# Optimization experiments

Hardware: AMD Instinct MI355X
Metric: run time of the kernel (lower is better)

## Reference

```python
import jax, jax.numpy as jnp
import numpy as np

B, N, FD, D, KS, NR, H, ITERS, L = 64, 1024, 768, 256, 8, 4, 4, 3, 2
TS = KS + NR          # total slots = 12
HD = D // H           # head dim = 64
SCALE = HD ** -0.5


def _ln(x, g, b):
    m = x.mean(-1, keepdims=True)
    v = ((x - m) ** 2).mean(-1, keepdims=True)
    return (x - m) / jnp.sqrt(v + 1e-5) * g + b


def setup_inputs() -> dict:
    key = jax.random.key(0)
    ks = iter(jax.random.split(key, 48))
    rn = lambda s, sc=0.02: jax.random.normal(next(ks), s, jnp.float32) * sc
    d = {}
    d['features'] = jax.random.normal(next(ks), (B, N, FD), jnp.float32)
    d['eps_noise'] = jax.random.normal(next(ks), (B, TS, D), jnp.float32)
    d['in_w'] = rn((FD, D)); d['in_b'] = jnp.zeros((D,))
    d['in_ln_g'] = jnp.ones((D,)); d['in_ln_b'] = jnp.zeros((D,))
    d['ni_g'] = jnp.ones((D,)); d['ni_b'] = jnp.zeros((D,))
    d['slot_mu'] = jax.random.normal(next(ks), (1, TS, D), jnp.float32) * D ** -0.5
    d['slot_log_sigma'] = jnp.zeros((1, TS, D), jnp.float32)
    d['q_w'] = rn((D, D)); d['k_w'] = rn((D, D)); d['v_w'] = rn((D, D))
    d['gru_wih'] = rn((D, 3 * D)); d['gru_whh'] = rn((D, 3 * D))
    d['gru_bih'] = jnp.zeros((3 * D,)); d['gru_bhh'] = jnp.zeros((3 * D,))
    d['ns_g'] = jnp.ones((D,)); d['ns_b'] = jnp.zeros((D,))
    d['ffn_ln_g'] = jnp.ones((D,)); d['ffn_ln_b'] = jnp.zeros((D,))
    d['ffn_w1'] = rn((D, 4 * D)); d['ffn_b1'] = jnp.zeros((4 * D,))
    d['ffn_w2'] = rn((4 * D, D)); d['ffn_b2'] = jnp.zeros((D,))
    d['sel_w1'] = rn((D, D // 2)); d['sel_b1'] = jnp.zeros((D // 2,))
    d['sel_w2'] = rn((D // 2, 2)); d['sel_b2'] = jnp.zeros((2,))
    d['gat_W'] = rn((L, D, D)); d['gat_a'] = rn((L, H, 2 * HD), 0.1)
    d['gat_ln_g'] = jnp.ones((L, D)); d['gat_ln_b'] = jnp.zeros((L, D))
    d['gat_fln_g'] = jnp.ones((L, D)); d['gat_fln_b'] = jnp.zeros((L, D))
    d['gat_fw1'] = rn((L, D, 4 * D)); d['gat_fb1'] = jnp.zeros((L, 4 * D))
    d['gat_fw2'] = rn((L, 4 * D, D)); d['gat_fb2'] = jnp.zeros((L, D))
    return d


def reference(features, eps_noise, in_w, in_b, in_ln_g, in_ln_b, ni_g, ni_b,
              slot_mu, slot_log_sigma, q_w, k_w, v_w,
              gru_wih, gru_whh, gru_bih, gru_bhh, ns_g, ns_b,
              ffn_ln_g, ffn_ln_b, ffn_w1, ffn_b1, ffn_w2, ffn_b2,
              sel_w1, sel_b1, sel_w2, sel_b2,
              gat_W, gat_a, gat_ln_g, gat_ln_b, gat_fln_g, gat_fln_b,
              gat_fw1, gat_fb1, gat_fw2, gat_fb2):
    # ---- slot attention ----
    inputs = _ln(features @ in_w + in_b, in_ln_g, in_ln_b)
    x_n = _ln(inputs, ni_g, ni_b)
    slots = slot_mu + jnp.exp(slot_log_sigma) * eps_noise          # [B,TS,D]
    k = (x_n @ k_w).reshape(B, N, H, HD)
    v = (x_n @ v_w).reshape(B, N, H, HD)
    for _ in range(ITERS):
        sn = _ln(slots, ns_g, ns_b)
        q = (sn @ q_w).reshape(B, TS, H, HD)
        dots = jnp.einsum('bihd,bjhd->bihj', q, k) * SCALE         # [B,TS,H,N]
        attn = jax.nn.softmax(dots.reshape(B, TS * H, N), axis=1).reshape(B, TS, H, N)
        attn_n = (attn + 1e-8) / (attn.sum(-1, keepdims=True) + 1e-8)
        updates = jnp.einsum('bjhd,bihj->bihd', v, attn_n).reshape(B * TS, D)
        h_prev = slots.reshape(B * TS, D)
        gx = updates @ gru_wih + gru_bih
        gh = h_prev @ gru_whh + gru_bhh
        xr, xz, xn = jnp.split(gx, 3, axis=-1)
        hr, hz, hn = jnp.split(gh, 3, axis=-1)
        r = jax.nn.sigmoid(xr + hr)
        z = jax.nn.sigmoid(xz + hz)
        n_ = jnp.tanh(xn + r * hn)
        slots = ((1 - z) * n_ + z * h_prev).reshape(B, TS, D)
        f = _ln(slots, ffn_ln_g, ffn_ln_b)
        slots = slots + jax.nn.gelu(f @ ffn_w1 + ffn_b1, approximate=False) @ ffn_w2 + ffn_b2
    obj = slots[:, :KS]
    # ---- slot selection (eval path: argmax) ----
    logits = jax.nn.relu(obj @ sel_w1 + sel_b1) @ sel_w2 + sel_b2  # [B,KS,2]
    decision = (jnp.argmax(logits, -1) == 1).astype(jnp.float32)
    needed = jnp.maximum(2.0 - decision.sum(-1), 0.0)
    inact = 1.0 - decision
    rank = jnp.cumsum(inact, -1)
    decision = jnp.where((inact > 0) & (rank <= needed[:, None]), 1.0, decision)
    x = obj * decision[..., None]
    # ---- GAT reasoning over slots ----
    mask2d = decision[:, :, None] * decision[:, None, :]           # [B,KS,KS]
    for l in range(L):
        hmat = (_ln(x, gat_ln_g[l], gat_ln_b[l]) @ gat_W[l]).reshape(B, KS, H, HD)
        ei = jnp.einsum('bkhd,hd->bkh', hmat, gat_a[l][:, :HD])
        ej = jnp.einsum('bkhd,hd->bkh', hmat, gat_a[l][:, HD:])
        e = ei[:, :, :, None] + jnp.transpose(ej, (0, 2, 1))[:, None, :, :]  # [B,K,H,K]
        e = jnp.where(e >= 0, e, 0.2 * e)
        e = jnp.where(mask2d[:, :, None, :] == 0, -1e9, e)
        alpha = jax.nn.softmax(e, axis=-1)
        out = jnp.einsum('bkhn,bnhd->bkhd', alpha, hmat).reshape(B, KS, D)
        y = x + out
        f = _ln(y, gat_fln_g[l], gat_fln_b[l])
        x = y + jax.nn.gelu(f @ gat_fw1[l] + gat_fb1[l], approximate=False) @ gat_fw2[l] + gat_fb2[l]
    return x
```

## Files before the change

kernel.cpp:

```cpp
#include <hip/hip_runtime.h>
#include <math.h>

#define Bb 64
#define Nn 1024
#define FDd 768
#define Dd 256
#define KSs 8
#define TSs 12
#define Hh 4
#define HDd 64

typedef __attribute__((ext_vector_type(8))) short bf16x8;
typedef __attribute__((ext_vector_type(4))) float f32x4;

__device__ __forceinline__ ushort f2bf(float x) {
    union { float f; uint u; } v; v.f = x;
    uint r = v.u + 0x7FFFu + ((v.u >> 16) & 1u);
    return (ushort)(r >> 16);
}
__device__ __forceinline__ float bf2f(ushort x) {
    union { uint u; float f; } v; v.u = ((uint)x) << 16;
    return v.f;
}
__device__ __forceinline__ uint pack2(float a, float b) {
    return (uint)f2bf(a) | ((uint)f2bf(b) << 16);
}
__device__ __forceinline__ float waveSum(float v) {
    #pragma unroll
    for (int o = 32; o > 0; o >>= 1) v += __shfl_xor(v, o);
    return v;
}
__device__ __forceinline__ float geluf(float v) {
    return 0.5f * v * (1.f + erff(v * 0.70710678118654752f));
}
__device__ __forceinline__ float sigm(float x) { return 1.f / (1.f + expf(-x)); }

__device__ __forceinline__ void load_af(bf16x8* af, const ushort* Alds, int lda, int lr, int lk)
{
    #pragma unroll
    for (int c = 0; c < 8; c++)
        af[c] = *(const bf16x8*)(Alds + lr * lda + c * 32 + lk * 8);
}

template<int NT, typename F>
__device__ __forceinline__ void mm_stream256(const bf16x8* af,
    const ushort* __restrict__ WT, int n0, int lr, int lk, F&& emit)
{
    const ushort* base = WT + (size_t)(n0 + lr) * 256 + lk * 8;
    bf16x8 bA[8], bB[8], bC[8];
    #pragma unroll
    for (int c = 0; c < 8; c++) bA[c] = *(const bf16x8*)(base + c * 32);
    if (NT > 1) {
        const ushort* nb = base + (size_t)16 * 256;
        #pragma unroll
        for (int c = 0; c < 8; c++) bB[c] = *(const bf16x8*)(nb + c * 32);
    }
    #pragma unroll
    for (int nt = 0; nt < NT; nt++) {
        const bf16x8* bc = (nt % 3 == 0) ? bA : (nt % 3 == 1) ? bB : bC;
        bf16x8* bn = (nt % 3 == 0) ? bC : (nt % 3 == 1) ? bA : bB;
        if (nt + 2 < NT) {
            const ushort* nb = base + (size_t)(nt + 2) * 16 * 256;
            #pragma unroll
            for (int c = 0; c < 8; c++) bn[c] = *(const bf16x8*)(nb + c * 32);
        }
        f32x4 a0 = {0.f, 0.f, 0.f, 0.f}, a1 = {0.f, 0.f, 0.f, 0.f};
        #pragma unroll
        for (int c = 0; c < 8; c += 2) a0 = __builtin_amdgcn_mfma_f32_16x16x32_bf16(af[c], bc[c], a0, 0, 0, 0);
        #pragma unroll
        for (int c = 1; c < 8; c += 2) a1 = __builtin_amdgcn_mfma_f32_16x16x32_bf16(af[c], bc[c], a1, 0, 0, 0);
        emit(nt, a0 + a1);
    }
}

template<int NT2, typename F>
__device__ __forceinline__ void mm_stream_1024(const ushort* Alds, int lda,
    const ushort* __restrict__ WT, int n0, int lr, int lk, F&& emit)
{
    f32x4 acc[NT2] = {};
    bf16x8 bA[8], bB[8], bC[8];
    {
        const ushort* nb = WT + (size_t)(n0 + lr) * 1024 + lk * 8;
        #pragma unroll
        for (int c = 0; c < 8; c++) bA[c] = *(const bf16x8*)(nb + c * 32);
    }
    if (4 * NT2 > 1) {
        const int kc1 = 1 / NT2, nt1 = 1 % NT2;
        const ushort* nb = WT + (size_t)(n0 + nt1 * 16 + lr) * 1024 + kc1 * 256 + lk * 8;
        #pragma unroll
        for (int c = 0; c < 8; c++) bB[c] = *(const bf16x8*)(nb + c * 32);
    }
    #pragma unroll
    for (int kc = 0; kc < 4; kc++) {
        bf16x8 af[8];
        #pragma unroll
        for (int c = 0; c < 8; c++)
            af[c] = *(const bf16x8*)(Alds + lr * lda + kc * 256 + c * 32 + lk * 8);
        #pragma unroll
        for (int nt = 0; nt < NT2; nt++) {
            const int step = kc * NT2 + nt;
            const bf16x8* bc = (step % 3 == 0) ? bA : (step % 3 == 1) ? bB : bC;
            bf16x8* bn = (step % 3 == 0) ? bC : (step % 3 == 1) ? bA : bB;
            if (step + 2 < 4 * NT2) {
                const int kc2 = (step + 2) / NT2, nt2 = (step + 2) % NT2;
                const ushort* nb = WT + (size_t)(n0 + nt2 * 16 + lr) * 1024 + kc2 * 256 + lk * 8;
                #pragma unroll
                for (int c = 0; c < 8; c++) bn[c] = *(const bf16x8*)(nb + c * 32);
            }
            #pragma unroll
            for (int c = 0; c < 8; c++)
                acc[nt] = __builtin_amdgcn_mfma_f32_16x16x32_bf16(af[c], bc[c], acc[nt], 0, 0, 0);
        }
    }
    #pragma unroll
    for (int nt = 0; nt < NT2; nt++) emit(nt, acc[nt]);
}

__device__ __forceinline__ void ln_row_bf(const float* __restrict__ rowF,
    ushort* __restrict__ rowU, const float* __restrict__ g,
    const float* __restrict__ b, int lane)
{
    float4 x = *(const float4*)&rowF[lane * 4];
    float m = waveSum(x.x + x.y + x.z + x.w) * (1.f / 256.f);
    float d0 = x.x - m, d1 = x.y - m, d2 = x.z - m, d3 = x.w - m;
    float v = waveSum(d0 * d0 + d1 * d1 + d2 * d2 + d3 * d3) * (1.f / 256.f);
    float inv = 1.f / sqrtf(v + 1e-5f);
    float4 gg = *(const float4*)&g[lane * 4];
    float4 bb = *(const float4*)&b[lane * 4];
    ushort4 o;
    o.x = f2bf(d0 * inv * gg.x + bb.x); o.y = f2bf(d1 * inv * gg.y + bb.y);
    o.z = f2bf(d2 * inv * gg.z + bb.z); o.w = f2bf(d3 * inv * gg.w + bb.w);
    *(ushort4*)&rowU[lane * 4] = o;
}

#define LPAD 40
template<bool A_F32, bool DO_LN>
__global__ __launch_bounds__(256) void gemm_mfma(const void* __restrict__ Ap,
    const ushort* __restrict__ WTa, const ushort* __restrict__ WTb,
    const float* __restrict__ bias,
    const float* __restrict__ g1, const float* __restrict__ b1,
    const float* __restrict__ g2, const float* __restrict__ b2,
    ushort* __restrict__ Ca, ushort* __restrict__ Cb, int M, int K)
{
    constexpr int SMEM_USHORTS = DO_LN ? (64 * 264) : (64 * LPAD + 256 * LPAD);
    __shared__ __align__(16) ushort smem[SMEM_USHORTS];
    ushort* As = smem;
    ushort* Bs = smem + 64 * LPAD;
    ushort* xS = smem;
    const ushort* WT = blockIdx.y ? WTb : WTa;
    ushort* C = blockIdx.y ? Cb : Ca;
    const int t = threadIdx.x;
    const int m0 = blockIdx.x * 64;
    const int lane = t & 63, wv = t >> 6;
    const int lr = lane & 15, lk = lane >> 4;

    f32x4 acc[4][4] = {};

    const float*  agf = (const float*)Ap  + (size_t)(m0 + (t >> 2)) * K + (t & 3) * 8;
    const ushort* agb = (const ushort*)Ap + (size_t)(m0 + (t >> 2)) * K + (t & 3) * 8;
    const ushort* bg  = WT + (size_t)(t >> 2) * K + (t & 3) * 8;

    float4 fA0, fA1; int4 iA0; int4 iB0, iB1, iB2, iB3;

#define GLOAD(k0) do { \
        if (A_F32) { \
            fA0 = *(const float4*)(agf + (k0)); fA1 = *(const float4*)(agf + (k0) + 4); \
        } else { \
            iA0 = *(const int4*)(agb + (k0)); \
        } \
        iB0 = *(const int4*)(bg + (k0)); \
        iB1 = *(const int4*)(bg + (size_t)64  * K + (k0)); \
        iB2 = *(const int4*)(bg + (size_t)128 * K + (k0)); \
        iB3 = *(const int4*)(bg + (size_t)192 * K + (k0)); \
    } while (0)

#define LSTORE() do { \
        if (A_F32) { \
            int4 w; \
            w.x = pack2(fA0.x, fA0.y); w.y = pack2(fA0.z, fA0.w); \
            w.z = pack2(fA1.x, fA1.y); w.w = pack2(fA1.z, fA1.w); \
            *(int4*)&As[(t >> 2) * LPAD + (t & 3) * 8] = w; \
        } else { \
            *(int4*)&As[(t >> 2) * LPAD + (t & 3) * 8] = iA0; \
        } \
        *(int4*)&Bs[(t >> 2) * LPAD + (t & 3) * 8]         = iB0; \
        *(int4*)&Bs[(64 + (t >> 2)) * LPAD + (t & 3) * 8]  = iB1; \
        *(int4*)&Bs[(128 + (t >> 2)) * LPAD + (t & 3) * 8] = iB2; \
        *(int4*)&Bs[(192 + (t >> 2)) * LPAD + (t & 3) * 8] = iB3; \
    } while (0)

    GLOAD(0);
    for (int k0 = 0; k0 < K; k0 += 32) {
        LSTORE();
        __syncthreads();
        bf16x8 af[4], bfr[4];
        #pragma unroll
        for (int mi = 0; mi < 4; mi++)
            af[mi] = *(const bf16x8*)&As[(mi * 16 + lr) * LPAD + lk * 8];
        #pragma unroll
        for (int ni = 0; ni < 4; ni++)
            bfr[ni] = *(const bf16x8*)&Bs[(wv * 64 + ni * 16 + lr) * LPAD + lk * 8];
        if (k0 + 32 < K) GLOAD(k0 + 32);
        #pragma unroll
        for (int mi = 0; mi < 4; mi++)
            #pragma unroll
            for (int ni = 0; ni < 4; ni++)
                acc[mi][ni] = __builtin_amdgcn_mfma_f32_16x16x32_bf16(af[mi], bfr[ni], acc[mi][ni], 0, 0, 0);
        __syncthreads();
    }
#undef GLOAD
#undef LSTORE
    if (DO_LN) {
        #pragma unroll
        for (int mi = 0; mi < 4; mi++) {
            int row = mi * 16 + lk * 4;
            #pragma unroll
            for (int ni = 0; ni < 4; ni++) {
                int col = wv * 64 + ni * 16 + lr;
                float bv = bias[col];
                #pragma unroll
                for (int r = 0; r < 4; r++)
                    xS[(row + r) * 264 + col] = f2bf(acc[mi][ni][r] + bv);
            }
        }
        __syncthreads();
        #pragma unroll
        for (int rr = 0; rr < 16; rr++) {
            int row = wv * 16 + rr;
            ushort4 u = *(const ushort4*)&xS[row * 264 + lane * 4];
            float x0 = bf2f(u.x), x1 = bf2f(u.y), x2 = bf2f(u.z), x3 = bf2f(u.w);
            float m = waveSum(x0 + x1 + x2 + x3) * (1.f / 256.f);
            float d0 = x0 - m, d1 = x1 - m, d2 = x2 - m, d3 = x3 - m;
            float v = waveSum(d0 * d0 + d1 * d1 + d2 * d2 + d3 * d3) * (1.f / 256.f);
            float inv = 1.f / sqrtf(v + 1e-5f);
            float4 gg = *(const float4*)&g1[lane * 4];
            float4 bbv = *(const float4*)&b1[lane * 4];
            float y0 = d0 * inv * gg.x + bbv.x, y1 = d1 * inv * gg.y + bbv.y;
            float y2 = d2 * inv * gg.z + bbv.z, y3 = d3 * inv * gg.w + bbv.w;
            float m2 = waveSum(y0 + y1 + y2 + y3) * (1.f / 256.f);
            float e0 = y0 - m2, e1 = y1 - m2, e2 = y2 - m2, e3 = y3 - m2;
            float v2 = waveSum(e0 * e0 + e1 * e1 + e2 * e2 + e3 * e3) * (1.f / 256.f);
            float inv2 = 1.f / sqrtf(v2 + 1e-5f);
            float4 g2v = *(const float4*)&g2[lane * 4];
            float4 b2v = *(const float4*)&b2[lane * 4];
            ushort4 o;
            o.x = f2bf(e0 * inv2 * g2v.x + b2v.x); o.y = f2bf(e1 * inv2 * g2v.y + b2v.y);
            o.z = f2bf(e2 * inv2 * g2v.z + b2v.z); o.w = f2bf(e3 * inv2 * g2v.w + b2v.w);
            *(ushort4*)&xS[row * 264 + lane * 4] = o;
        }
        __syncthreads();
        for (int idx = t; idx < 4096; idx += 256) {
            int row = idx >> 6, cg = (idx & 63) * 4;
            *(ushort4*)&C[(size_t)(m0 + row) * 256 + cg] =
                *(const ushort4*)&xS[row * 264 + cg];
        }
    } else {
        #pragma unroll
        for (int mi = 0; mi < 4; mi++) {
            int grow = m0 + mi * 16 + lk * 4;
            #pragma unroll
            for (int ni = 0; ni < 4; ni++) {
                int gcol = wv * 64 + ni * 16 + lr;
                float bv = bias ? bias[gcol] : 0.f;
                #pragma unroll
                for (int r = 0; r < 4; r++)
                    C[(size_t)(grow + r) * 256 + gcol] = f2bf(acc[mi][ni][r] + bv);
            }
        }
    }
}

struct PrepArgsT {
    const float* src[14];
    ushort* dst[14];
    int K[14];
    int N[14];
    int tstart[15];
};
__global__ __launch_bounds__(256) void prep_tiled(PrepArgsT pa)
{
    __shared__ float s[32][33];
    int tile = blockIdx.x;
    int seg = 0;
    while (tile >= pa.tstart[seg + 1]) seg++;
    int lt = tile - pa.tstart[seg];
    int K = pa.K[seg], N = pa.N[seg];
    int tpr = N >> 5;
    int k0 = (lt / tpr) << 5, n0 = (lt % tpr) << 5;
    const float* src = pa.src[seg];
    ushort* dst = pa.dst[seg];
    int r = threadIdx.x >> 5, c = threadIdx.x & 31;
    #pragma unroll
    for (int rr = 0; rr < 32; rr += 8)
        s[rr + r][c] = src[(size_t)(k0 + rr + r) * N + n0 + c];
    __syncthreads();
    #pragma unroll
    for (int rr = 0; rr < 32; rr += 8)
        dst[(size_t)(n0 + rr + r) * K + k0 + c] = f2bf(s[c][rr + r]);
}

__global__ __launch_bounds__(512) void slot_init_q(
    const float* __restrict__ mu, const float* __restrict__ ls,
    const float* __restrict__ eps, float* __restrict__ slots_g,
    float* __restrict__ qbuf, const ushort* __restrict__ qwT,
    const float* __restrict__ ns_g, const float* __restrict__ ns_b)
{
    __shared__ float sF[16 * 256];
    __shared__ __align__(16) ushort sU[16 * 264];
    int b = blockIdx.x, t = threadIdx.x;
    int lane = t & 63, wv = t >> 6, lr = lane & 15, lk = lane >> 4;
    for (int idx = t; idx < 4096; idx += 512) {
        int i = idx >> 8, c = idx & 255;
        float v = 0.f;
        if (i < 12) {
            int md = i * 256 + c;
            v = mu[md] + expf(ls[md]) * eps[(size_t)(b * 12 + i) * 256 + c];
            slots_g[(size_t)(b * 12 + i) * 256 + c] = v;
        }
        sF[idx] = v;
        sU[i * 264 + c] = 0;
    }
    __syncthreads();
    ln_row_bf(sF + wv * 256, sU + wv * 264, ns_g, ns_b, lane);
    if (wv < 4) ln_row_bf(sF + (8 + wv) * 256, sU + (8 + wv) * 264, ns_g, ns_b, lane);
    __syncthreads();
    bf16x8 af[8];
    load_af(af, sU, 264, lr, lk);
    mm_stream256<2>(af, qwT, wv * 32, lr, lk, [&](int nt, f32x4 a) {
        int n = wv * 32 + nt * 16 + lr;
        #pragma unroll
        for (int r = 0; r < 4; r++) {
            int m = lk * 4 + r;
            if (m < 12) qbuf[(size_t)(b * 12 + m) * 256 + n] = a[r] * 0.125f;
        }
    });
}

__global__ __launch_bounds__(256) void dots_softmax(const float* __restrict__ qb,
    const ushort* __restrict__ kb, ushort* __restrict__ attnb)
{
    int b = blockIdx.x >> 2, chunk = blockIdx.x & 3;
    int t = threadIdx.x;
    int j = chunk * 256 + t;
    const float* qbase = qb + (size_t)b * 12 * 256;
    float a48[48];
    #pragma unroll
    for (int h = 0; h < 4; h++) {
        const uint* kp = (const uint*)(kb + (size_t)(b * Nn + j) * 256 + h * 64);
        float kr[64];
        #pragma unroll
        for (int c = 0; c < 8; c++) {
            int4 k4 = *(const int4*)(kp + c * 4);
            uint u0 = (uint)k4.x, u1 = (uint)k4.y, u2 = (uint)k4.z, u3 = (uint)k4.w;
            kr[c * 8 + 0] = __uint_as_float(u0 << 16); kr[c * 8 + 1] = __uint_as_float(u0 & 0xffff0000u);
            kr[c * 8 + 2] = __uint_as_float(u1 << 16); kr[c * 8 + 3] = __uint_as_float(u1 & 0xffff0000u);
            kr[c * 8 + 4] = __uint_as_float(u2 << 16); kr[c * 8 + 5] = __uint_as_float(u2 & 0xffff0000u);
            kr[c * 8 + 6] = __uint_as_float(u3 << 16); kr[c * 8 + 7] = __uint_as_float(u3 & 0xffff0000u);
        }
        #pragma unroll
        for (int i = 0; i < 12; i++) {
            const float* qr = qbase + i * 256 + h * 64;
            float acc = 0.f;
            #pragma unroll
            for (int c = 0; c < 64; c++) acc += kr[c] * qr[c];
            a48[i * 4 + h] = acc;
        }
    }
    float m = -1e30f;
    #pragma unroll
    for (int idx = 0; idx < 48; idx++) m = fmaxf(m, a48[idx]);
    float s = 0.f;
    #pragma unroll
    for (int idx = 0; idx < 48; idx++) { a48[idx] = expf(a48[idx] - m); s += a48[idx]; }
    float inv = 1.f / s;
    #pragma unroll
    for (int idx = 0; idx < 48; idx++)
        attnb[(size_t)(b * 48 + idx) * Nn + j] = f2bf(a48[idx] * inv);
}

__global__ __launch_bounds__(512) void updates_kernel(const ushort* __restrict__ attnb,
    const ushort* __restrict__ vb, float* __restrict__ upd)
{
    int b = blockIdx.x >> 2, h = blockIdx.x & 3;
    int t = threadIdx.x, w = t >> 6, lane = t & 63;
    int jj = lane >> 3, dg = lane & 7;
    float acc[12][8] = {};
    float ra[12] = {};
    float accv[8] = {};
    for (int jb = w * 8; jb < Nn; jb += 64) {
        int j = jb + jj;
        bf16x8 v8 = *(const bf16x8*)&vb[(size_t)(b * Nn + j) * Dd + h * HDd + dg * 8];
        float vv[8];
        #pragma unroll
        for (int r = 0; r < 8; r++) { vv[r] = bf2f((ushort)v8[r]); accv[r] += vv[r]; }
        #pragma unroll
        for (int i = 0; i < 12; i++) {
            float a = bf2f(attnb[(size_t)(b * 48 + i * 4 + h) * Nn + j]);
            #pragma unroll
            for (int r = 0; r < 8; r++) acc[i][r] += a * vv[r];
            ra[i] += a;
        }
    }
    #pragma unroll
    for (int i = 0; i < 12; i++) {
        #pragma unroll
        for (int r = 0; r < 8; r++) {
            acc[i][r] += __shfl_xor(acc[i][r], 8);
            acc[i][r] += __shfl_xor(acc[i][r], 16);
            acc[i][r] += __shfl_xor(acc[i][r], 32);
        }
        ra[i] += __shfl_xor(ra[i], 8);
        ra[i] += __shfl_xor(ra[i], 16);
        ra[i] += __shfl_xor(ra[i], 32);
    }
    #pragma unroll
    for (int r = 0; r < 8; r++) {
        accv[r] += __shfl_xor(accv[r], 8);
        accv[r] += __shfl_xor(accv[r], 16);
        accv[r] += __shfl_xor(accv[r], 32);
    }
    __shared__ float redA[8][12][64];
    __shared__ float redV[8][64];
    __shared__ float redR[8][12];
    if (lane < 8) {
        #pragma unroll
        for (int i = 0; i < 12; i++)
            #pragma unroll
            for (int r = 0; r < 8; r++)
                redA[w][i][lane * 8 + r] = acc[i][r];
        #pragma unroll
        for (int r = 0; r < 8; r++) redV[w][lane * 8 + r] = accv[r];
        if (lane == 0) {
            #pragma unroll
            for (int i = 0; i < 12; i++) redR[w][i] = ra[i];
        }
    }
    __syncthreads();
    if (w == 0) {
        float sv = 0.f;
        #pragma unroll
        for (int ww = 0; ww < 8; ww++) sv += redV[ww][lane];
        #pragma unroll
        for (int i = 0; i < 12; i++) {
            float s = 0.f, rs = 0.f;
            #pragma unroll
            for (int ww = 0; ww < 8; ww++) { s += redA[ww][i][lane]; rs += redR[ww][i]; }
            upd[(size_t)(b * TSs + i) * Dd + h * HDd + lane] = (s + 1e-8f * sv) / (rs + 1e-8f);
        }
    }
}

__global__ __launch_bounds__(256) void gru_mm(const float* __restrict__ upd,
    const float* __restrict__ slots_g,
    const ushort* __restrict__ wihT, const ushort* __restrict__ whhT,
    const float* __restrict__ bih, const float* __restrict__ bhh,
    float* __restrict__ gxh)
{
    __shared__ __align__(16) ushort sU[16 * 264], sS[16 * 264];
    int b = blockIdx.x, q = blockIdx.y, t = threadIdx.x;
    int lane = t & 63, wv = t >> 6, lr = lane & 15, lk = lane >> 4;
    for (int idx = t; idx < 4096; idx += 256) {
        int i = idx >> 8, c = idx & 255;
        float uv = 0.f, sv = 0.f;
        if (i < 12) {
            uv = upd[(size_t)(b * 12 + i) * 256 + c];
            sv = slots_g[(size_t)(b * 12 + i) * 256 + c];
        }
        sU[i * 264 + c] = f2bf(uv);
        sS[i * 264 + c] = f2bf(sv);
    }
    __syncthreads();
    bool ih = (wv < 2);
    bf16x8 af[8];
    load_af(af, ih ? sU : sS, 264, lr, lk);
    const ushort* W = ih ? wihT : whhT;
    const float* bias = ih ? bih : bhh;
    float* outp = gxh + (size_t)(b * 2 + (ih ? 0 : 1)) * 12 * 768;
    int n0 = q * 192 + (wv & 1) * 96;
    mm_stream256<6>(af, W, n0, lr, lk, [&](int nt, f32x4 a) {
        int n = n0 + nt * 16 + lr;
        float bv = bias[n];
        #pragma unroll
        for (int r = 0; r < 4; r++) {
            int m = lk * 4 + r;
            if (m < 12) outp[m * 768 + n] = a[r] + bv;
        }
    });
}

__global__ __launch_bounds__(256) void gate_ffn1(const float* __restrict__ gxh,
    const float* __restrict__ slots_g, float* __restrict__ slots2,
    const ushort* __restrict__ fw1T,
    const float* __restrict__ fln_g, const float* __restrict__ fln_b,
    const float* __restrict__ f_b1, ushort* __restrict__ h1b)
{
    __shared__ float sF[12 * 256];
    __shared__ __align__(16) ushort sU[16 * 264];
    int b = blockIdx.x, q = blockIdx.y, t = threadIdx.x;
    int lane = t & 63, wv = t >> 6, lr = lane & 15, lk = lane >> 4;
    for (int idx = t; idx < 1056; idx += 256) sU[12 * 264 + idx] = 0;
    for (int idx = t; idx < 3072; idx += 256) {
        int i = idx >> 8, c = idx & 255;
        const float* gx = gxh + (size_t)(b * 2) * 12 * 768 + i * 768;
        const float* gh = gxh + (size_t)(b * 2 + 1) * 12 * 768 + i * 768;
        float r = sigm(gx[c] + gh[c]);
        float z = sigm(gx[256 + c] + gh[256 + c]);
        float nv = tanhf(gx[512 + c] + r * gh[512 + c]);
        float hp = slots_g[(size_t)(b * 12 + i) * 256 + c];
        float out = (1.f - z) * nv + z * hp;
        sF[idx] = out;
        if (q == 0) slots2[(size_t)(b * 12 + i) * 256 + c] = out;
    }
    __syncthreads();
    for (int rr = 0; rr < 3; rr++) {
        int row = wv * 3 + rr;
        ln_row_bf(sF + row * 256, sU + row * 264, fln_g, fln_b, lane);
    }
    __syncthreads();
    bf16x8 af[8];
    load_af(af, sU, 264, lr, lk);
    int n0 = q * 256 + wv * 64;
    mm_stream256<4>(af, fw1T, n0, lr, lk, [&](int nt, f32x4 a) {
        int n = n0 + nt * 16 + lr;
        float bv = f_b1[n];
        #pragma unroll
        for (int r = 0; r < 4; r++) {
            int m = lk * 4 + r;
            if (m < 12) h1b[(size_t)(b * 12 + m) * 1024 + n] = f2bf(geluf(a[r] + bv));
        }
    });
}

__global__ __launch_bounds__(256) void ffn2_mm(const ushort* __restrict__ h1b,
    const float* __restrict__ slots2, float* __restrict__ slots_g,
    const ushort* __restrict__ fw2T, const float* __restrict__ f_b2)
{
    __shared__ __align__(16) ushort hS[16 * 1032];
    int b = blockIdx.x, q = blockIdx.y, t = threadIdx.x;
    int lane = t & 63, wv = t >> 6, lr = lane & 15, lk = lane >> 4;
    for (int ch = t; ch < 2048; ch += 256) {
        int i = ch >> 7, c8 = (ch & 127) * 8;
        int4 v = {0, 0, 0, 0};
        if (i < 12) v = *(const int4*)&h1b[(size_t)(b * 12 + i) * 1024 + c8];
        *(int4*)&hS[i * 1032 + c8] = v;
    }
    __syncthreads();
    int n0 = q * 64 + wv * 16;
    mm_stream_1024<1>(hS, 1032, fw2T, n0, lr, lk, [&](int nt, f32x4 a) {
        (void)nt;
        int n = n0 + lr;
        float bv = f_b2[n];
        #pragma unroll
        for (int r = 0; r < 4; r++) {
            int m = lk * 4 + r;
            if (m < 12)
                slots_g[(size_t)(b * 12 + m) * 256 + n] =
                    a[r] + bv + slots2[(size_t)(b * 12 + m) * 256 + n];
        }
    });
}

__global__ __launch_bounds__(512) void ln_q(const float* __restrict__ slots_g,
    float* __restrict__ qbuf, const ushort* __restrict__ qwT,
    const float* __restrict__ ns_g, const float* __restrict__ ns_b)
{
    __shared__ float sF[12 * 256];
    __shared__ __align__(16) ushort sU[16 * 264];
    int b = blockIdx.x, t = threadIdx.x;
    int lane = t & 63, wv = t >> 6, lr = lane & 15, lk = lane >> 4;
    for (int idx = t; idx < 3072; idx += 512) sF[idx] = slots_g[(size_t)b * 3072 + idx];
    for (int idx = t; idx < 1056; idx += 512) sU[12 * 264 + idx] = 0;
    __syncthreads();
    ln_row_bf(sF + wv * 256, sU + wv * 264, ns_g, ns_b, lane);
    if (wv < 4) ln_row_bf(sF + (8 + wv) * 256, sU + (8 + wv) * 264, ns_g, ns_b, lane);
    __syncthreads();
    bf16x8 af[8];
    load_af(af, sU, 264, lr, lk);
    mm_stream256<2>(af, qwT, wv * 32, lr, lk, [&](int nt, f32x4 a) {
        int n = wv * 32 + nt * 16 + lr;
        #pragma unroll
        for (int r = 0; r < 4; r++) {
            int m = lk * 4 + r;
            if (m < 12) qbuf[(size_t)(b * 12 + m) * 256 + n] = a[r] * 0.125f;
        }
    });
}

__global__ __launch_bounds__(256) void select_kernel(const float* __restrict__ slots,
    const float* __restrict__ w1, const float* __restrict__ b1,
    const float* __restrict__ w2, const float* __restrict__ b2,
    float* __restrict__ dec, float* __restrict__ xout)
{
    int b = blockIdx.x, t = threadIdx.x;
    __shared__ float t1[8][128];
    __shared__ float lg[8][2];
    __shared__ float dsh[8];
    const float* obj = slots + (size_t)b * TSs * Dd;
    #pragma unroll
    for (int u = 0; u < 4; u++) {
        int idx = t + 256 * u;
        int k = idx >> 7, c = idx & 127;
        float s = b1[c];
        for (int d = 0; d < 256; d++) s += obj[k * 256 + d] * w1[d * 128 + c];
        t1[k][c] = fmaxf(s, 0.f);
    }
    __syncthreads();
    if (t < 16) {
        int k = t >> 1, o = t & 1;
        float s = b2[o];
        for (int c = 0; c < 128; c++) s += t1[k][c] * w2[c * 2 + o];
        lg[k][o] = s;
    }
    __syncthreads();
    if (t == 0) {
        float dv[8]; float sum = 0.f;
        for (int k = 0; k < 8; k++) { dv[k] = (lg[k][1] > lg[k][0]) ? 1.f : 0.f; sum += dv[k]; }
        float needed = fmaxf(2.f - sum, 0.f);
        float rank = 0.f;
        for (int k = 0; k < 8; k++) {
            float inact = 1.f - dv[k];
            rank += inact;
            if (inact > 0.f && rank <= needed) dv[k] = 1.f;
            dsh[k] = dv[k];
            dec[b * 8 + k] = dv[k];
        }
    }
    __syncthreads();
    for (int idx = t; idx < 2048; idx += 256) {
        int k = idx >> 8, c = idx & 255;
        xout[(size_t)(b * 8 + k) * 256 + c] = obj[k * 256 + c] * dsh[k];
    }
}

__global__ __launch_bounds__(256) void gat_attn(const float* __restrict__ xin,
    const float* __restrict__ dec, const ushort* __restrict__ gWT,
    const float* __restrict__ av,
    const float* __restrict__ lng, const float* __restrict__ lnb,
    const float* __restrict__ flng, const float* __restrict__ flnb,
    float* __restrict__ yF, ushort* __restrict__ ylnb)
{
    __shared__ float xF[8 * 256];
    __shared__ float hmF[8 * 256];
    __shared__ __align__(16) ushort sU[16 * 264];
    __shared__ float ei[8][4], ej[8][4], al[8][4][8], ds[8];
    int b = blockIdx.x, t = threadIdx.x;
    int lane = t & 63, wv = t >> 6, lr = lane & 15, lk = lane >> 4;

    for (int idx = t; idx < 2048; idx += 256) xF[idx] = xin[(size_t)b * 2048 + idx];
    for (int idx = t; idx < 2112; idx += 256) sU[8 * 264 + idx] = 0;
    if (t < 8) ds[t] = dec[b * 8 + t];
    __syncthreads();
    ln_row_bf(xF + (wv * 2) * 256, sU + (wv * 2) * 264, lng, lnb, lane);
    ln_row_bf(xF + (wv * 2 + 1) * 256, sU + (wv * 2 + 1) * 264, lng, lnb, lane);
    __syncthreads();
    {
        bf16x8 af[8];
        load_af(af, sU, 264, lr, lk);
        mm_stream256<4>(af, gWT, wv * 64, lr, lk, [&](int nt, f32x4 a) {
            int n = wv * 64 + nt * 16 + lr;
            #pragma unroll
            for (int r = 0; r < 4; r++) {
                int m = lk * 4 + r;
                if (m < 8) hmF[m * 256 + n] = a[r];
            }
        });
    }
    __syncthreads();
    {
        int pair = t >> 3, sub = t & 7;
        int k = pair >> 2, h = pair & 3;
        const float* hrow = hmF + k * 256 + h * 64 + sub * 8;
        float s1 = 0.f, s2 = 0.f;
        #pragma unroll
        for (int d = 0; d < 8; d++) {
            float hv = hrow[d];
            s1 += hv * av[h * 128 + sub * 8 + d];
            s2 += hv * av[h * 128 + 64 + sub * 8 + d];
        }
        #pragma unroll
        for (int o = 1; o < 8; o <<= 1) { s1 += __shfl_xor(s1, o); s2 += __shfl_xor(s2, o); }
        if (sub == 0) { ei[k][h] = s1; ej[k][h] = s2; }
    }
    __syncthreads();
    {
        int k = t >> 5, h = (t >> 3) & 3, n = t & 7;
        float e = ei[k][h] + ej[n][h];
        e = (e >= 0.f) ? e : 0.2f * e;
        if (ds[k] * ds[n] == 0.f) e = -1e9f;
        float mx = e;
        #pragma unroll
        for (int o = 4; o > 0; o >>= 1) mx = fmaxf(mx, __shfl_xor(mx, o, 8));
        float ex = expf(e - mx);
        float sm = ex;
        #pragma unroll
        for (int o = 4; o > 0; o >>= 1) sm += __shfl_xor(sm, o, 8);
        al[k][h][n] = ex / sm;
    }
    __syncthreads();
    {
        int h = t >> 6, d = t & 63;
        #pragma unroll
        for (int k = 0; k < 8; k++) {
            float o = 0.f;
            #pragma unroll
            for (int n = 0; n < 8; n++) o += al[k][h][n] * hmF[n * 256 + h * 64 + d];
            xF[k * 256 + h * 64 + d] += o;
        }
    }
    __syncthreads();
    for (int idx = t; idx < 2048; idx += 256) yF[(size_t)b * 2048 + idx] = xF[idx];
    ln_row_bf(xF + (wv * 2) * 256, sU + (wv * 2) * 264, flng, flnb, lane);
    ln_row_bf(xF + (wv * 2 + 1) * 256, sU + (wv * 2 + 1) * 264, flng, flnb, lane);
    __syncthreads();
    for (int idx = t; idx < 2048; idx += 256) {
        int i = idx >> 8, c = idx & 255;
        ylnb[(size_t)b * 2048 + idx] = sU[i * 264 + c];
    }
}

__global__ __launch_bounds__(256) void gat_ffn1(const ushort* __restrict__ ylnb,
    const ushort* __restrict__ g1T, const float* __restrict__ fb1,
    ushort* __restrict__ gh1)
{
    __shared__ __align__(16) ushort sU[16 * 264];
    int b = blockIdx.x, q = blockIdx.y, t = threadIdx.x;
    int lane = t & 63, wv = t >> 6, lr = lane & 15, lk = lane >> 4;
    for (int idx = t; idx < 4096; idx += 256) {
        int i = idx >> 8, c = idx & 255;
        sU[i * 264 + c] = (i < 8) ? ylnb[(size_t)b * 2048 + i * 256 + c] : 0;
    }
    __syncthreads();
    bf16x8 af[8];
    load_af(af, sU, 264, lr, lk);
    int n0 = q * 256 + wv * 64;
    mm_stream256<4>(af, g1T, n0, lr, lk, [&](int nt, f32x4 a) {
        int n = n0 + nt * 16 + lr;
        float bv = fb1[n];
        #pragma unroll
        for (int r = 0; r < 4; r++) {
            int m = lk * 4 + r;
            if (m < 8) gh1[(size_t)(b * 8 + m) * 1024 + n] = f2bf(geluf(a[r] + bv));
        }
    });
}

__global__ __launch_bounds__(256) void gat_ffn2(const ushort* __restrict__ gh1,
    const float* __restrict__ yF, const ushort* __restrict__ g2T,
    const float* __restrict__ fb2, float* __restrict__ out)
{
    __shared__ __align__(16) ushort hS[16 * 1032];
    int b = blockIdx.x, q = blockIdx.y, t = threadIdx.x;
    int lane = t & 63, wv = t >> 6, lr = lane & 15, lk = lane >> 4;
    for (int ch = t; ch < 2048; ch += 256) {
        int i = ch >> 7, c8 = (ch & 127) * 8;
        int4 v = {0, 0, 0, 0};
        if (i < 8) v = *(const int4*)&gh1[(size_t)(b * 8 + i) * 1024 + c8];
        *(int4*)&hS[i * 1032 + c8] = v;
    }
    __syncthreads();
    int n0 = q * 64 + wv * 16;
    mm_stream_1024<1>(hS, 1032, g2T, n0, lr, lk, [&](int nt, f32x4 a) {
        (void)nt;
        int n = n0 + lr;
        float bv = fb2[n];
        #pragma unroll
        for (int r = 0; r < 4; r++) {
            int m = lk * 4 + r;
            if (m < 8) out[(size_t)(b * 8 + m) * 256 + n] = a[r] + bv + yF[(size_t)(b * 8 + m) * 256 + n];
        }
    });
}

extern "C" void kernel_launch(void* const* d_in, const int* in_sizes, int n_in,
                              void* d_out, int out_size, void* d_ws, size_t ws_size,
                              hipStream_t stream)
{
    (void)in_sizes; (void)n_in; (void)out_size; (void)ws_size;
    const float* features       = (const float*)d_in[0];
    const float* eps_noise      = (const float*)d_in[1];
    const float* in_w           = (const float*)d_in[2];
    const float* in_b           = (const float*)d_in[3];
    const float* in_ln_g        = (const float*)d_in[4];
    const float* in_ln_b        = (const float*)d_in[5];
    const float* ni_g           = (const float*)d_in[6];
    const float* ni_b           = (const float*)d_in[7];
    const float* slot_mu        = (const float*)d_in[8];
    const float* slot_log_sigma = (const float*)d_in[9];
    const float* q_w            = (const float*)d_in[10];
    const float* k_w            = (const float*)d_in[11];
    const float* v_w            = (const float*)d_in[12];
    const float* gru_wih        = (const float*)d_in[13];
    const float* gru_whh        = (const float*)d_in[14];
    const float* gru_bih        = (const float*)d_in[15];
    const float* gru_bhh        = (const float*)d_in[16];
    const float* ns_g           = (const float*)d_in[17];
    const float* ns_b           = (const float*)d_in[18];
    const float* ffn_ln_g       = (const float*)d_in[19];
    const float* ffn_ln_b       = (const float*)d_in[20];
    const float* ffn_w1         = (const float*)d_in[21];
    const float* ffn_b1         = (const float*)d_in[22];
    const float* ffn_w2         = (const float*)d_in[23];
    const float* ffn_b2         = (const float*)d_in[24];
    const float* sel_w1         = (const float*)d_in[25];
    const float* sel_b1         = (const float*)d_in[26];
    const float* sel_w2         = (const float*)d_in[27];
    const float* sel_b2         = (const float*)d_in[28];
    const float* gat_W          = (const float*)d_in[29];
    const float* gat_a          = (const float*)d_in[30];
    const float* gat_ln_g       = (const float*)d_in[31];
    const float* gat_ln_b       = (const float*)d_in[32];
    const float* gat_fln_g      = (const float*)d_in[33];
    const float* gat_fln_b      = (const float*)d_in[34];
    const float* gat_fw1        = (const float*)d_in[35];
    const float* gat_fb1        = (const float*)d_in[36];
    const float* gat_fw2        = (const float*)d_in[37];
    const float* gat_fb2        = (const float*)d_in[38];

    ushort* kb  = (ushort*)d_ws;
    ushort* vb  = kb + 16777216;
    ushort* xnb = vb + 16777216;
    ushort* wtb = xnb + 16777216;
    ushort* h1b  = wtb + 2490368;
    ushort* ylnb = h1b + 786432;
    ushort* gh1  = ylnb + 131072;
    ushort* attnb = gh1 + 524288;
    float* fbase = (float*)(attnb + 3145728);
    float* slots  = fbase;
    float* slots2 = slots + 196608;
    float* qbuf   = slots2 + 196608;
    float* upd    = qbuf + 196608;
    float* gxh    = upd + 196608;
    float* xb     = gxh + 1179648;
    float* yF     = xb + 131072;
    float* dec    = yF + 131072;

    ushort* in_wT = wtb;
    ushort* k_wT  = in_wT + 196608;
    ushort* v_wT  = k_wT + 65536;
    ushort* q_wT  = v_wT + 65536;
    ushort* wihT  = q_wT + 65536;
    ushort* whhT  = wihT + 196608;
    ushort* fw1T  = whhT + 196608;
    ushort* fw2T  = fw1T + 262144;
    ushort* gW0T  = fw2T + 262144;
    ushort* gW1T  = gW0T + 65536;
    ushort* gf1aT = gW1T + 65536;
    ushort* gf1bT = gf1aT + 262144;
    ushort* gf2aT = gf1bT + 262144;
    ushort* gf2bT = gf2aT + 262144;

    dim3 blk(256);

    PrepArgsT pa;
    const float* srcs[14] = { in_w, k_w, v_w, q_w, gru_wih, gru_whh, ffn_w1, ffn_w2,
                              gat_W, gat_W + 65536, gat_fw1, gat_fw1 + 262144,
                              gat_fw2, gat_fw2 + 262144 };
    ushort* dsts[14] = { in_wT, k_wT, v_wT, q_wT, wihT, whhT, fw1T, fw2T,
                         gW0T, gW1T, gf1aT, gf1bT, gf2aT, gf2bT };
    int Ks[14]  = { 768, 256, 256, 256, 256, 256, 256, 1024, 256, 256, 256, 256, 1024, 1024 };
    int Nsz[14] = { 256, 256, 256, 256, 768, 768, 1024, 256, 256, 256, 1024, 1024, 256, 256 };
    int tcum = 0;
    for (int s = 0; s < 14; s++) {
        pa.src[s] = srcs[s]; pa.dst[s] = dsts[s]; pa.K[s] = Ks[s]; pa.N[s] = Nsz[s];
        pa.tstart[s] = tcum;
        tcum += (Ks[s] >> 5) * (Nsz[s] >> 5);
    }
    pa.tstart[14] = tcum;
    prep_tiled<<<tcum, blk, 0, stream>>>(pa);

    gemm_mfma<true, true><<<dim3(1024, 1), blk, 0, stream>>>(
        features, in_wT, nullptr, in_b, in_ln_g, in_ln_b, ni_g, ni_b,
        xnb, nullptr, Bb * Nn, 768);

    gemm_mfma<false, false><<<dim3(1024, 2), blk, 0, stream>>>(
        xnb, k_wT, v_wT, nullptr, nullptr, nullptr, nullptr, nullptr,
        kb, vb, Bb * Nn, 256);

    slot_init_q<<<Bb, dim3(512), 0, stream>>>(slot_mu, slot_log_sigma, eps_noise,
                                              slots, qbuf, q_wT, ns_g, ns_b);

    for (int it = 0; it < 3; it++) {
        dots_softmax<<<Bb * 4, blk, 0, stream>>>(qbuf, kb, attnb);
        updates_kernel<<<Bb * Hh, dim3(512), 0, stream>>>(attnb, vb, upd);
        gru_mm<<<dim3(Bb, 4), blk, 0, stream>>>(upd, slots, wihT, whhT,
                                                gru_bih, gru_bhh, gxh);
        gate_ffn1<<<dim3(Bb, 4), blk, 0, stream>>>(gxh, slots, slots2, fw1T,
                                                   ffn_ln_g, ffn_ln_b, ffn_b1, h1b);
        ffn2_mm<<<dim3(Bb, 4), blk, 0, stream>>>(h1b, slots2, slots, fw2T, ffn_b2);
        if (it < 2)
            ln_q<<<Bb, dim3(512), 0, stream>>>(slots, qbuf, q_wT, ns_g, ns_b);
    }

    select_kernel<<<Bb, blk, 0, stream>>>(slots, sel_w1, sel_b1, sel_w2, sel_b2, dec, xb);

    for (int l = 0; l < 2; l++) {
        const ushort* gWT = l ? gW1T : gW0T;
        const ushort* g1T = l ? gf1bT : gf1aT;
        const ushort* g2T = l ? gf2bT : gf2aT;
        gat_attn<<<Bb, blk, 0, stream>>>(xb, dec, gWT, gat_a + l * 512,
            gat_ln_g + l * 256, gat_ln_b + l * 256,
            gat_fln_g + l * 256, gat_fln_b + l * 256, yF, ylnb);
        gat_ffn1<<<dim3(Bb, 4), blk, 0, stream>>>(ylnb, g1T, gat_fb1 + l * 1024, gh1);
        gat_ffn2<<<dim3(Bb, 4), blk, 0, stream>>>(gh1, yF, g2T, gat_fb2 + l * 256,
            l ? (float*)d_out : xb);
    }
}
```

Before: 567.0 us.

## Fuse input projection, double layernorm, and K/V projections into one kernel

The input-projection GEMM with its two layernorms and the K/V projection GEMM now run in a single kernel. The normalized 64x256 tile stays in shared memory and is multiplied directly by the K and V weights, which are read from global memory with register double-buffering. This removes the round trip of the normalized activation buffer through global memory and one kernel launch. In exchange, each block re-streams the full K and V weight matrices without LDS staging, and register pressure rises.

```diff
diff --git a/kernel.cpp b/kernel.cpp
--- a/kernel.cpp
+++ b/kernel.cpp
@@ -134,21 +134,19 @@
 }
 
 #define LPAD 40
-template<bool A_F32, bool DO_LN>
-__global__ __launch_bounds__(256) void gemm_mfma(const void* __restrict__ Ap,
-    const ushort* __restrict__ WTa, const ushort* __restrict__ WTb,
+__global__ __launch_bounds__(256) void inproj_kv(const float* __restrict__ Ap,
+    const ushort* __restrict__ WT,
+    const ushort* __restrict__ kwT, const ushort* __restrict__ vwT,
     const float* __restrict__ bias,
     const float* __restrict__ g1, const float* __restrict__ b1,
     const float* __restrict__ g2, const float* __restrict__ b2,
-    ushort* __restrict__ Ca, ushort* __restrict__ Cb, int M, int K)
-{
-    constexpr int SMEM_USHORTS = DO_LN ? (64 * 264) : (64 * LPAD + 256 * LPAD);
-    __shared__ __align__(16) ushort smem[SMEM_USHORTS];
+    ushort* __restrict__ kb, ushort* __restrict__ vb)
+{
+    constexpr int K = 768;
+    __shared__ __align__(16) ushort smem[64 * 264];
     ushort* As = smem;
     ushort* Bs = smem + 64 * LPAD;
     ushort* xS = smem;
-    const ushort* WT = blockIdx.y ? WTb : WTa;
-    ushort* C = blockIdx.y ? Cb : Ca;
     const int t = threadIdx.x;
     const int m0 = blockIdx.x * 64;
     const int lane = t & 63, wv = t >> 6;
@@ -156,18 +154,13 @@
 
     f32x4 acc[4][4] = {};
 
-    const float*  agf = (const float*)Ap  + (size_t)(m0 + (t >> 2)) * K + (t & 3) * 8;
-    const ushort* agb = (const ushort*)Ap + (size_t)(m0 + (t >> 2)) * K + (t & 3) * 8;
+    const float*  agf = Ap + (size_t)(m0 + (t >> 2)) * K + (t & 3) * 8;
     const ushort* bg  = WT + (size_t)(t >> 2) * K + (t & 3) * 8;
 
-    float4 fA0, fA1; int4 iA0; int4 iB0, iB1, iB2, iB3;
+    float4 fA0, fA1; int4 iB0, iB1, iB2, iB3;
 
 #define GLOAD(k0) do { \
-        if (A_F32) { \
-            fA0 = *(const float4*)(agf + (k0)); fA1 = *(const float4*)(agf + (k0) + 4); \
-        } else { \
-            iA0 = *(const int4*)(agb + (k0)); \
-        } \
+        fA0 = *(const float4*)(agf + (k0)); fA1 = *(const float4*)(agf + (k0) + 4); \
         iB0 = *(const int4*)(bg + (k0)); \
         iB1 = *(const int4*)(bg + (size_t)64  * K + (k0)); \
         iB2 = *(const int4*)(bg + (size_t)128 * K + (k0)); \
@@ -175,14 +168,10 @@
     } while (0)
 
 #define LSTORE() do { \
-        if (A_F32) { \
-            int4 w; \
-            w.x = pack2(fA0.x, fA0.y); w.y = pack2(fA0.z, fA0.w); \
-            w.z = pack2(fA1.x, fA1.y); w.w = pack2(fA1.z, fA1.w); \
-            *(int4*)&As[(t >> 2) * LPAD + (t & 3) * 8] = w; \
-        } else { \
-            *(int4*)&As[(t >> 2) * LPAD + (t & 3) * 8] = iA0; \
-        } \
+        int4 w; \
+        w.x = pack2(fA0.x, fA0.y); w.y = pack2(fA0.z, fA0.w); \
+        w.z = pack2(fA1.x, fA1.y); w.w = pack2(fA1.z, fA1.w); \
+        *(int4*)&As[(t >> 2) * LPAD + (t & 3) * 8] = w; \
         *(int4*)&Bs[(t >> 2) * LPAD + (t & 3) * 8]         = iB0; \
         *(int4*)&Bs[(64 + (t >> 2)) * LPAD + (t & 3) * 8]  = iB1; \
         *(int4*)&Bs[(128 + (t >> 2)) * LPAD + (t & 3) * 8] = iB2; \
@@ -210,62 +199,73 @@
     }
 #undef GLOAD
 #undef LSTORE
-    if (DO_LN) {
-        #pragma unroll
-        for (int mi = 0; mi < 4; mi++) {
-            int row = mi * 16 + lk * 4;
-            #pragma unroll
-            for (int ni = 0; ni < 4; ni++) {
-                int col = wv * 64 + ni * 16 + lr;
-                float bv = bias[col];
+    #pragma unroll
+    for (int mi = 0; mi < 4; mi++) {
+        int row = mi * 16 + lk * 4;
+        #pragma unroll
+        for (int ni = 0; ni < 4; ni++) {
+            int col = wv * 64 + ni * 16 + lr;
+            float bv = bias[col];
+            #pragma unroll
+            for (int r = 0; r < 4; r++)
+                xS[(row + r) * 264 + col] = f2bf(acc[mi][ni][r] + bv);
+        }
+    }
+    __syncthreads();
+    #pragma unroll
+    for (int rr = 0; rr < 16; rr++) {
+        int row = wv * 16 + rr;
+        ushort4 u = *(const ushort4*)&xS[row * 264 + lane * 4];
+        float x0 = bf2f(u.x), x1 = bf2f(u.y), x2 = bf2f(u.z), x3 = bf2f(u.w);
+        float m = waveSum(x0 + x1 + x2 + x3) * (1.f / 256.f);
+        float d0 = x0 - m, d1 = x1 - m, d2 = x2 - m, d3 = x3 - m;
+        float v = waveSum(d0 * d0 + d1 * d1 + d2 * d2 + d3 * d3) * (1.f / 256.f);
+        float inv = 1.f / sqrtf(v + 1e-5f);
+        float4 gg = *(const float4*)&g1[lane * 4];
+        float4 bbv = *(const float4*)&b1[lane * 4];
+        float y0 = d0 * inv * gg.x + bbv.x, y1 = d1 * inv * gg.y + bbv.y;
+        float y2 = d2 * inv * gg.z + bbv.z, y3 = d3 * inv * gg.w + bbv.w;
+        float m2 = waveSum(y0 + y1 + y2 + y3) * (1.f / 256.f);
+        float e0 = y0 - m2, e1 = y1 - m2, e2 = y2 - m2, e3 = y3 - m2;
+        float v2 = waveSum(e0 * e0 + e1 * e1 + e2 * e2 + e3 * e3) * (1.f / 256.f);
+        float inv2 = 1.f / sqrtf(v2 + 1e-5f);
+        float4 g2v = *(const float4*)&g2[lane * 4];
+        float4 b2v = *(const float4*)&b2[lane * 4];
+        ushort4 o;
+        o.x = f2bf(e0 * inv2 * g2v.x + b2v.x); o.y = f2bf(e1 * inv2 * g2v.y + b2v.y);
+        o.z = f2bf(e2 * inv2 * g2v.z + b2v.z); o.w = f2bf(e3 * inv2 * g2v.w + b2v.w);
+        *(ushort4*)&xS[row * 264 + lane * 4] = o;
+    }
+    __syncthreads();
+    bf16x8 af2[8];
+    load_af(af2, xS + (wv * 16) * 264, 264, lr, lk);
+    #pragma unroll
+    for (int wsel = 0; wsel < 2; wsel++) {
+        const ushort* W = wsel ? vwT : kwT;
+        ushort* outp = wsel ? vb : kb;
+        bf16x8 bufA[8], bufB[8];
+        {
+            const ushort* nb = W + (size_t)lr * 256 + lk * 8;
+            #pragma unroll
+            for (int c = 0; c < 8; c++) bufA[c] = *(const bf16x8*)(nb + c * 32);
+        }
+        #pragma unroll
+        for (int nt = 0; nt < 16; nt++) {
+            const bf16x8* cur = (nt & 1) ? bufB : bufA;
+            bf16x8* nxt = (nt & 1) ? bufA : bufB;
+            if (nt + 1 < 16) {
+                const ushort* nb = W + (size_t)((nt + 1) * 16 + lr) * 256 + lk * 8;
                 #pragma unroll
-                for (int r = 0; r < 4; r++)
-                    xS[(row + r) * 264 + col] = f2bf(acc[mi][ni][r] + bv);
+                for (int c = 0; c < 8; c++) nxt[c] = *(const bf16x8*)(nb + c * 32);
             }
-        }
-        __syncthreads();
-        #pragma unroll
-        for (int rr = 0; rr < 16; rr++) {
-            int row = wv * 16 + rr;
-            ushort4 u = *(const ushort4*)&xS[row * 264 + lane * 4];
-            float x0 = bf2f(u.x), x1 = bf2f(u.y), x2 = bf2f(u.z), x3 = bf2f(u.w);
-            float m = waveSum(x0 + x1 + x2 + x3) * (1.f / 256.f);
-            float d0 = x0 - m, d1 = x1 - m, d2 = x2 - m, d3 = x3 - m;
-            float v = waveSum(d0 * d0 + d1 * d1 + d2 * d2 + d3 * d3) * (1.f / 256.f);
-            float inv = 1.f / sqrtf(v + 1e-5f);
-            float4 gg = *(const float4*)&g1[lane * 4];
-            float4 bbv = *(const float4*)&b1[lane * 4];
-            float y0 = d0 * inv * gg.x + bbv.x, y1 = d1 * inv * gg.y + bbv.y;
-            float y2 = d2 * inv * gg.z + bbv.z, y3 = d3 * inv * gg.w + bbv.w;
-            float m2 = waveSum(y0 + y1 + y2 + y3) * (1.f / 256.f);
-            float e0 = y0 - m2, e1 = y1 - m2, e2 = y2 - m2, e3 = y3 - m2;
-            float v2 = waveSum(e0 * e0 + e1 * e1 + e2 * e2 + e3 * e3) * (1.f / 256.f);
-            float inv2 = 1.f / sqrtf(v2 + 1e-5f);
-            float4 g2v = *(const float4*)&g2[lane * 4];
-            float4 b2v = *(const float4*)&b2[lane * 4];
-            ushort4 o;
-            o.x = f2bf(e0 * inv2 * g2v.x + b2v.x); o.y = f2bf(e1 * inv2 * g2v.y + b2v.y);
-            o.z = f2bf(e2 * inv2 * g2v.z + b2v.z); o.w = f2bf(e3 * inv2 * g2v.w + b2v.w);
-            *(ushort4*)&xS[row * 264 + lane * 4] = o;
-        }
-        __syncthreads();
-        for (int idx = t; idx < 4096; idx += 256) {
-            int row = idx >> 6, cg = (idx & 63) * 4;
-            *(ushort4*)&C[(size_t)(m0 + row) * 256 + cg] =
-                *(const ushort4*)&xS[row * 264 + cg];
-        }
-    } else {
-        #pragma unroll
-        for (int mi = 0; mi < 4; mi++) {
-            int grow = m0 + mi * 16 + lk * 4;
-            #pragma unroll
-            for (int ni = 0; ni < 4; ni++) {
-                int gcol = wv * 64 + ni * 16 + lr;
-                float bv = bias ? bias[gcol] : 0.f;
-                #pragma unroll
-                for (int r = 0; r < 4; r++)
-                    C[(size_t)(grow + r) * 256 + gcol] = f2bf(acc[mi][ni][r] + bv);
-            }
+            f32x4 a = {0.f, 0.f, 0.f, 0.f};
+            #pragma unroll
+            for (int c = 0; c < 8; c++)
+                a = __builtin_amdgcn_mfma_f32_16x16x32_bf16(af2[c], cur[c], a, 0, 0, 0);
+            int n = nt * 16 + lr;
+            #pragma unroll
+            for (int r = 0; r < 4; r++)
+                outp[(size_t)(m0 + wv * 16 + lk * 4 + r) * 256 + n] = f2bf(a[r]);
         }
     }
 }
@@ -868,13 +868,8 @@
     pa.tstart[14] = tcum;
     prep_tiled<<<tcum, blk, 0, stream>>>(pa);
 
-    gemm_mfma<true, true><<<dim3(1024, 1), blk, 0, stream>>>(
-        features, in_wT, nullptr, in_b, in_ln_g, in_ln_b, ni_g, ni_b,
-        xnb, nullptr, Bb * Nn, 768);
-
-    gemm_mfma<false, false><<<dim3(1024, 2), blk, 0, stream>>>(
-        xnb, k_wT, v_wT, nullptr, nullptr, nullptr, nullptr, nullptr,
-        kb, vb, Bb * Nn, 256);
+    inproj_kv<<<1024, blk, 0, stream>>>(features, in_wT, k_wT, v_wT, in_b,
+                                        in_ln_g, in_ln_b, ni_g, ni_b, kb, vb);
 
     slot_init_q<<<Bb, dim3(512), 0, stream>>>(slot_mu, slot_log_sigma, eps_noise,
                                               slots, qbuf, q_wT, ns_g, ns_b);
```

Measured after the change: 629.8 us. 1.11x slower.
